# Performance work log

Measured on AMD Instinct MI355X. Metric: run time of the kernel, lower is better.

## Reference

```python
import jax, jax.numpy as jnp
import numpy as np

B, N, S = 2, 16384, 4096
C_FEAT = 6
RADII = (0.5, 1.0)
NSAMPLES = (16, 32)
MLPS = ([9, 16, 16, 32], [9, 32, 32, 64])  # in-channels = 3 (xyz) + 6 (features)
IC, PC, OUT = 64, 96, 128  # image ch, point ch (32+64), fusion out
RC = PC // 4


def _w(key, o, i):
    return jax.random.normal(key, (o, i), jnp.float32) / np.sqrt(i)


def setup_inputs() -> dict:
    key = jax.random.key(0)
    ks = jax.random.split(key, 40)
    inp = {
        "xyz": jax.random.normal(ks[0], (B, N, 3), jnp.float32),
        "features": jax.random.normal(ks[1], (B, C_FEAT, N), jnp.float32),
        "img_features": jax.random.normal(ks[2], (B, IC, S), jnp.float32),
    }
    k = 3
    for s, mlp in enumerate(MLPS):
        for l in range(len(mlp) - 1):
            inp[f"w{s}_{l}"] = _w(ks[k], mlp[l + 1], mlp[l]); k += 1
            inp[f"b{s}_{l}"] = jnp.zeros((mlp[l + 1],), jnp.float32)
    inp["w_img"] = _w(ks[k], PC, IC); k += 1
    inp["b_img"] = jnp.zeros((PC,), jnp.float32)
    inp["w_fc2"] = _w(ks[k], RC, PC); k += 1
    inp["b_fc2"] = jnp.zeros((RC,), jnp.float32)
    inp["w_fc3"] = _w(ks[k], 1, RC); k += 1
    inp["b_fc3"] = jnp.zeros((1,), jnp.float32)
    inp["w_pc"] = _w(ks[k], PC, PC); k += 1
    inp["b_pc"] = jnp.zeros((PC,), jnp.float32)
    inp["w_fuse"] = _w(ks[k], OUT, 2 * PC); k += 1
    inp["b_fuse"] = jnp.zeros((OUT,), jnp.float32)
    return inp


def conv1d(w, b, x):
    # 1x1 Conv1d: w [O,C], x [B,C,N]
    return jnp.einsum('oc,bcn->bon', w, x) + b[None, :, None]


def fps(xyz, npoint):
    # farthest point sampling. xyz: [B,N,3] -> idx [B,npoint]
    b, n, _ = xyz.shape
    first = jnp.zeros((b,), jnp.int32)

    def body(carry, _):
        dists, last = carry
        last_xyz = jnp.take_along_axis(xyz, last[:, None, None].astype(jnp.int32), axis=1)  # [B,1,3]
        d = jnp.sum((xyz - last_xyz) ** 2, -1)  # [B,N]
        dists = jnp.minimum(dists, d)
        nxt = jnp.argmax(dists, -1).astype(jnp.int32)
        return (dists, nxt), nxt

    (_, _), rest = jax.lax.scan(body, (jnp.full((b, n), 1e10, jnp.float32), first), None, length=npoint - 1)
    return jnp.concatenate([first[None, :], rest], 0).T  # [B,npoint]


def ball_query(xyz, new_xyz, radius, nsample):
    # xyz [B,N,3], new_xyz [B,S,3] -> idx [B,S,nsample]
    d2 = jnp.sum((new_xyz[:, :, None, :] - xyz[:, None, :, :]) ** 2, -1)  # [B,S,N]
    ar = jnp.arange(xyz.shape[1], dtype=jnp.int32)
    keys = jnp.where(d2 < radius * radius, ar[None, None, :], xyz.shape[1])
    idx = -jax.lax.top_k(-keys, nsample)[0]  # nsample smallest keys (first in-ball indices)
    first = idx[..., :1]
    idx = jnp.where(idx == xyz.shape[1], first, idx)  # pad with first in-ball index (pointnet2 semantics)
    return jnp.minimum(idx, xyz.shape[1] - 1)


def _forward(xyz, features, img_features, params):
    (w0_0, b0_0, w0_1, b0_1, w0_2, b0_2,
     w1_0, b1_0, w1_1, b1_1, w1_2, b1_2,
     w_img, b_img, w_fc2, b_fc2, w_fc3, b_fc3, w_pc, b_pc, w_fuse, b_fuse) = params
    layers = [[(w0_0, b0_0), (w0_1, b0_1), (w0_2, b0_2)],
              [(w1_0, b1_0), (w1_1, b1_1), (w1_2, b1_2)]]

    fps_idx = fps(xyz, S)  # [B,S]
    new_xyz = jnp.take_along_axis(xyz, fps_idx[:, :, None], axis=1)  # [B,S,3]

    outs = []
    for radius, nsample, mlp in zip(RADII, NSAMPLES, layers):
        idx = ball_query(xyz, new_xyz, radius, nsample)  # [B,S,K]
        g_xyz = jax.vmap(lambda p, i: p[i])(xyz, idx)  # [B,S,K,3]
        g_xyz = (g_xyz - new_xyz[:, :, None, :]).transpose(0, 3, 1, 2)  # [B,3,S,K]
        g_feat = jax.vmap(lambda f, i: f[:, i])(features, idx)  # [B,C,S,K]
        h = jnp.concatenate([g_xyz, g_feat], axis=1)  # [B,3+C,S,K]  (use_xyz)
        for w, b in mlp:
            h = jax.nn.relu(jnp.einsum('oc,bcsk->bosk', w, h) + b[None, :, None, None])
        outs.append(jnp.max(h, axis=-1))  # max-pool over neighborhood -> [B,Cout,S]
    point_feats = jnp.concatenate(outs, axis=1)  # [B,96,S]

    # IA_Layer (BatchNorm at default running stats ~ identity; omitted)
    img = jax.nn.relu(conv1d(w_img, b_img, img_features))  # [B,PC,S]
    flat = img.transpose(0, 2, 1)  # [B,S,PC]
    ri = jnp.tanh(flat @ w_fc2.T + b_fc2)  # [B,S,RC]
    att = jax.nn.sigmoid(ri @ w_fc3.T + b_fc3).transpose(0, 2, 1)  # [B,1,S]
    img_r = img + img * att
    img_new = jax.nn.relu(conv1d(w_pc, b_pc, img_r))  # [B,PC,S]

    fused = jnp.concatenate([point_feats, img_new], axis=1)  # [B,2*PC,S]
    return jax.nn.relu(conv1d(w_fuse, b_fuse, fused))  # [B,OUT,S]


def reference(xyz, features, img_features,
              w0_0, b0_0, w0_1, b0_1, w0_2, b0_2,
              w1_0, b1_0, w1_1, b1_1, w1_2, b1_2,
              w_img, b_img, w_fc2, b_fc2, w_fc3, b_fc3,
              w_pc, b_pc, w_fuse, b_fuse):
    params = (w0_0, b0_0, w0_1, b0_1, w0_2, b0_2,
              w1_0, b1_0, w1_1, b1_1, w1_2, b1_2,
              w_img, b_img, w_fc2, b_fc2, w_fc3, b_fc3, w_pc, b_pc, w_fuse, b_fuse)
    return _forward(xyz, features, img_features, params)
```

## Files before the change

kernel.cpp:

```cpp
#include <hip/hip_runtime.h>
#include <cstdint>

typedef unsigned long long u64;

static constexpr int BB = 2;
static constexpr int NN = 16384;
static constexpr int SS = 4096;

template <int CTRL>
__device__ __forceinline__ u64 dpp_max_step(u64 k) {
  int lo = (int)(unsigned)(k & 0xffffffffull);
  int hi = (int)(unsigned)(k >> 32);
  int slo = __builtin_amdgcn_update_dpp(0, lo, CTRL, 0xF, 0xF, true);
  int shi = __builtin_amdgcn_update_dpp(0, hi, CTRL, 0xF, 0xF, true);
  u64 o = ((u64)(unsigned)shi << 32) | (u64)(unsigned)slo;
  return (o > k) ? o : k;
}

__device__ __forceinline__ unsigned spread4(unsigned v) {
  return (v & 1u) | ((v & 2u) << 2) | ((v & 4u) << 4) | ((v & 8u) << 6);
}

__device__ __forceinline__ unsigned cell_of(float x, float y, float z) {
  int cx = (int)floorf((x + 4.f) * 2.f);
  int cy = (int)floorf((y + 4.f) * 2.f);
  int cz = (int)floorf((z + 4.f) * 2.f);
  cx = min(max(cx, 0), 15); cy = min(max(cy, 0), 15); cz = min(max(cz, 0), 15);
  return spread4((unsigned)cx) | (spread4((unsigned)cy) << 1) |
         (spread4((unsigned)cz) << 2);
}

__global__ __launch_bounds__(1024) void sort_kernel(
    const float* __restrict__ xyz, float4* __restrict__ spts)
{
  const int b = blockIdx.x;
  const float* X = xyz + (size_t)b * NN * 3;
  float4* SP = spts + (size_t)b * NN;
  const int t = threadIdx.x;
  const int lane = t & 63, wid = t >> 6;

  __shared__ unsigned h[4096];
  __shared__ unsigned wtot[16];
  for (int j = t; j < 4096; j += 1024) h[j] = 0;
  __syncthreads();

  for (int i = 0; i < 16; ++i) {
    int p = i * 1024 + t;
    atomicAdd(&h[cell_of(X[p * 3 + 0], X[p * 3 + 1], X[p * 3 + 2])], 1u);
  }
  __syncthreads();

  unsigned a0 = h[4 * t], a1 = h[4 * t + 1], a2 = h[4 * t + 2], a3 = h[4 * t + 3];
  unsigned s4 = a0 + a1 + a2 + a3;
  unsigned incl = s4;
  for (int off = 1; off < 64; off <<= 1) {
    unsigned v = (unsigned)__shfl_up((int)incl, off);
    if (lane >= off) incl += v;
  }
  if (lane == 63) wtot[wid] = incl;
  __syncthreads();
  if (t == 0) {
    unsigned run = 0;
    for (int j = 0; j < 16; ++j) { unsigned tm = wtot[j]; wtot[j] = run; run += tm; }
  }
  __syncthreads();
  unsigned ex = wtot[wid] + (incl - s4);
  h[4 * t] = ex; h[4 * t + 1] = ex + a0;
  h[4 * t + 2] = ex + a0 + a1; h[4 * t + 3] = ex + a0 + a1 + a2;
  __syncthreads();

  for (int i = 0; i < 16; ++i) {
    int p = i * 1024 + t;
    float x = X[p * 3 + 0], y = X[p * 3 + 1], z = X[p * 3 + 2];
    unsigned pos = atomicAdd(&h[cell_of(x, y, z)], 1u);
    SP[pos] = make_float4(x, y, z, __int_as_float(p));
  }
}

__global__ __launch_bounds__(1024) void fps_kernel(
    const float* __restrict__ xyz, const float4* __restrict__ spts,
    float* __restrict__ new_xyz)
{
  const int b = blockIdx.x;
  const float* X = xyz + (size_t)b * NN * 3;
  float* NX = new_xyz + (size_t)b * SS * 3;
  const float4* SP = spts + (size_t)b * NN;
  const int t = threadIdx.x;
  const int lane = t & 63, wid = t >> 6;
  const int g = lane & 3;
  const float4* WP = SP + wid * 1024;

  float x0, x1, x2, x3, x4, x5, x6, x7, x8, x9, x10, x11, x12, x13, x14, x15;
  float y0, y1, y2, y3, y4, y5, y6, y7, y8, y9, y10, y11, y12, y13, y14, y15;
  float z0, z1, z2, z3, z4, z5, z6, z7, z8, z9, z10, z11, z12, z13, z14, z15;
  unsigned n0, n1, n2, n3, n4, n5, n6, n7, n8, n9, n10, n11, n12, n13, n14, n15;
#define LOADSLOT(s)                                                           \
  { float4 P = WP[(s) * 64 + lane];                                           \
    x##s = P.x; y##s = P.y; z##s = P.z; n##s = ~__float_as_uint(P.w); }
  LOADSLOT(0)  LOADSLOT(1)  LOADSLOT(2)  LOADSLOT(3)
  LOADSLOT(4)  LOADSLOT(5)  LOADSLOT(6)  LOADSLOT(7)
  LOADSLOT(8)  LOADSLOT(9)  LOADSLOT(10) LOADSLOT(11)
  LOADSLOT(12) LOADSLOT(13) LOADSLOT(14) LOADSLOT(15)
#undef LOADSLOT

  float d0 = 1e10f, d1 = 1e10f, d2 = 1e10f, d3 = 1e10f,
        d4 = 1e10f, d5 = 1e10f, d6 = 1e10f, d7 = 1e10f,
        d8 = 1e10f, d9 = 1e10f, d10 = 1e10f, d11 = 1e10f,
        d12 = 1e10f, d13 = 1e10f, d14 = 1e10f, d15 = 1e10f;

  float bnx = 0.f, bny = 0.f, bnz = 0.f, bxx = 0.f, bxy = 0.f, bxz = 0.f;
#define SUBBOX(J, A, B, C, D)                                                 \
  {                                                                           \
    float mnx = fminf(fminf(x##A, x##B), fminf(x##C, x##D));                  \
    float mxx = fmaxf(fmaxf(x##A, x##B), fmaxf(x##C, x##D));                  \
    float mny = fminf(fminf(y##A, y##B), fminf(y##C, y##D));                  \
    float mxy = fmaxf(fmaxf(y##A, y##B), fmaxf(y##C, y##D));                  \
    float mnz = fminf(fminf(z##A, z##B), fminf(z##C, z##D));                  \
    float mxz = fmaxf(fmaxf(z##A, z##B), fmaxf(z##C, z##D));                  \
    for (int off = 1; off < 64; off <<= 1) {                                  \
      mnx = fminf(mnx, __shfl_xor(mnx, off));                                 \
      mxx = fmaxf(mxx, __shfl_xor(mxx, off));                                 \
      mny = fminf(mny, __shfl_xor(mny, off));                                 \
      mxy = fmaxf(mxy, __shfl_xor(mxy, off));                                 \
      mnz = fminf(mnz, __shfl_xor(mnz, off));                                 \
      mxz = fmaxf(mxz, __shfl_xor(mxz, off));                                 \
    }                                                                         \
    if (g == J) { bnx = mnx; bny = mny; bnz = mnz;                            \
                  bxx = mxx; bxy = mxy; bxz = mxz; }                          \
  }
  SUBBOX(0, 0, 1, 2, 3)
  SUBBOX(1, 4, 5, 6, 7)
  SUBBOX(2, 8, 9, 10, 11)
  SUBBOX(3, 12, 13, 14, 15)
#undef SUBBOX

  unsigned klo = 0u, khi = __float_as_uint(1e10f);

  __shared__ u64 s_part[2][16];
  int sel = 0;

  for (int it = 1; it < SS; ++it) {
    const float qx = X[sel * 3 + 0];
    const float qy = X[sel * 3 + 1];
    const float qz = X[sel * 3 + 2];
    if (t == 0) {
      NX[(it - 1) * 3 + 0] = qx;
      NX[(it - 1) * 3 + 1] = qy;
      NX[(it - 1) * 3 + 2] = qz;
    }

    float tx = fmaxf(fmaxf(__fsub_rn(bnx, qx), __fsub_rn(qx, bxx)), 0.f);
    float ty = fmaxf(fmaxf(__fsub_rn(bny, qy), __fsub_rn(qy, bxy)), 0.f);
    float tz = fmaxf(fmaxf(__fsub_rn(bnz, qz), __fsub_rn(qz, bxz)), 0.f);
    float lb2 = fmaf(tx, tx, fmaf(ty, ty, __fmul_rn(tz, tz)));
    u64 bm = __ballot(__fmul_rn(lb2, 0.99998474f) < __uint_as_float(khi));
    unsigned m = (unsigned)bm & 0xFu;

#define UPD1(S)                                                               \
    {                                                                         \
      float dx = __fsub_rn(x##S, qx);                                         \
      float dy = __fsub_rn(y##S, qy);                                         \
      float dz = __fsub_rn(z##S, qz);                                         \
      float dsq = __fadd_rn(__fadd_rn(__fmul_rn(dx, dx), __fmul_rn(dy, dy)),  \
                            __fmul_rn(dz, dz));                               \
      d##S = fminf(d##S, dsq);                                                \
      u64 kp = ((u64)__float_as_uint(d##S) << 32) | (u64)(n##S);              \
      if (kp > kb) kb = kp;                                                   \
    }
#define SUBUPD(J, A, B, C, D)                                                 \
    if (m & (1u << J)) {                                                      \
      u64 kb = 0;                                                             \
      UPD1(A) UPD1(B) UPD1(C) UPD1(D)                                         \
      kb = dpp_max_step<0x111>(kb);                                           \
      kb = dpp_max_step<0x112>(kb);                                           \
      kb = dpp_max_step<0x114>(kb);                                           \
      kb = dpp_max_step<0x118>(kb);                                           \
      kb = dpp_max_step<0x142>(kb);                                           \
      kb = dpp_max_step<0x143>(kb);                                           \
      unsigned nlo = (unsigned)__shfl((int)(unsigned)(kb & 0xffffffffull), 63);\
      unsigned nhi = (unsigned)__shfl((int)(unsigned)(kb >> 32), 63);         \
      if (g == J) { klo = nlo; khi = nhi; }                                   \
    }
    SUBUPD(0, 0, 1, 2, 3)
    SUBUPD(1, 4, 5, 6, 7)
    SUBUPD(2, 8, 9, 10, 11)
    SUBUPD(3, 12, 13, 14, 15)
#undef SUBUPD
#undef UPD1

    u64 kw = ((u64)khi << 32) | (u64)klo;
    kw = dpp_max_step<0xB1>(kw);
    kw = dpp_max_step<0x4E>(kw);

    const int pb = it & 1;
    if (lane == 63) s_part[pb][wid] = kw;
    __syncthreads();
    u64 kk = s_part[pb][lane & 15];
    kk = dpp_max_step<0x128>(kk);
    kk = dpp_max_step<0x124>(kk);
    kk = dpp_max_step<0x122>(kk);
    kk = dpp_max_step<0x121>(kk);
    sel = (int)(~(unsigned)(kk & 0xffffffffull));
    sel = __builtin_amdgcn_readfirstlane(sel);
  }
  if (t == 0) {
    NX[(SS - 1) * 3 + 0] = X[sel * 3 + 0];
    NX[(SS - 1) * 3 + 1] = X[sel * 3 + 1];
    NX[(SS - 1) * 3 + 2] = X[sel * 3 + 2];
  }
}

template <int NS>
__global__ __launch_bounds__(256) void ballq_kernel(
    const float* __restrict__ xyz, const float* __restrict__ new_xyz,
    int* __restrict__ out, float r2)
{
  const int q = blockIdx.x * 4 + (threadIdx.x >> 6);
  const int lane = threadIdx.x & 63;
  const int b = q >> 12;
  const float* X = xyz + (size_t)b * NN * 3;
  const float cx = new_xyz[q * 3 + 0];
  const float cy = new_xyz[q * 3 + 1];
  const float cz = new_xyz[q * 3 + 2];
  int* o = out + (size_t)q * NS;
  int base = 0;
  int firstIdx = 0x7fffffff;
  for (int c0 = 0; c0 < NN; c0 += 64) {
    const int p = c0 + lane;
    float dx = __fsub_rn(cx, X[p * 3 + 0]);
    float dy = __fsub_rn(cy, X[p * 3 + 1]);
    float dz = __fsub_rn(cz, X[p * 3 + 2]);
    float d2 = __fadd_rn(__fadd_rn(__fmul_rn(dx, dx), __fmul_rn(dy, dy)),
                         __fmul_rn(dz, dz));
    const bool inb = d2 < r2;
    const unsigned long long mm = __ballot(inb);
    if (inb) {
      int rank = base + (int)__popcll(mm & ((1ull << lane) - 1ull));
      if (rank < NS) {
        o[rank] = p;
        if (rank == 0) firstIdx = p;
      }
    }
    base += (int)__popcll(mm);
    if (base >= NS) break;
  }
#pragma unroll
  for (int off = 32; off >= 1; off >>= 1)
    firstIdx = min(firstIdx, __shfl_xor(firstIdx, off));
  for (int r = base + lane; r < NS; r += 64) o[r] = firstIdx;
}

template <int NS, int C1, int C2, int C3>
__global__ __launch_bounds__(256) void group_mlp_kernel(
    const float* __restrict__ xyz, const float* __restrict__ feat,
    const float* __restrict__ new_xyz, const int* __restrict__ idx,
    const float* __restrict__ w0, const float* __restrict__ b0,
    const float* __restrict__ w1, const float* __restrict__ b1,
    const float* __restrict__ w2, const float* __restrict__ b2,
    float* __restrict__ pf, int chOff)
{
  constexpr int QPB = 256 / NS;
  const int q = blockIdx.x * QPB + (int)(threadIdx.x / NS);
  const int k = (int)(threadIdx.x % NS);
  const int b = q >> 12;
  const int s = q & (SS - 1);
  const float* X = xyz + (size_t)b * NN * 3;
  const float* F = feat + (size_t)b * 6 * NN;
  const int p = idx[(size_t)q * NS + k];

  float in[9];
  in[0] = X[p * 3 + 0] - new_xyz[q * 3 + 0];
  in[1] = X[p * 3 + 1] - new_xyz[q * 3 + 1];
  in[2] = X[p * 3 + 2] - new_xyz[q * 3 + 2];
#pragma unroll
  for (int c = 0; c < 6; ++c) in[3 + c] = F[c * NN + p];

  float h1[C1];
#pragma unroll
  for (int oc = 0; oc < C1; ++oc) {
    float a = b0[oc];
#pragma unroll
    for (int c = 0; c < 9; ++c) a = fmaf(w0[oc * 9 + c], in[c], a);
    h1[oc] = fmaxf(a, 0.f);
  }
  float h2[C2];
#pragma unroll
  for (int oc = 0; oc < C2; ++oc) {
    float a = b1[oc];
#pragma unroll
    for (int c = 0; c < C1; ++c) a = fmaf(w1[oc * C1 + c], h1[c], a);
    h2[oc] = fmaxf(a, 0.f);
  }
#pragma unroll
  for (int oc = 0; oc < C3; ++oc) {
    float a = b2[oc];
#pragma unroll
    for (int c = 0; c < C2; ++c) a = fmaf(w2[oc * C2 + c], h2[c], a);
    float v = fmaxf(a, 0.f);
#pragma unroll
    for (int off = NS / 2; off >= 1; off >>= 1)
      v = fmaxf(v, __shfl_xor(v, off));
    if (k == 0) pf[(((size_t)b * 96) + chOff + oc) * SS + s] = v;
  }
}

__global__ __launch_bounds__(256) void img_fuse_kernel(
    const float* __restrict__ imgf, const float* __restrict__ pf,
    const float* __restrict__ w_img, const float* __restrict__ b_img,
    const float* __restrict__ w_fc2, const float* __restrict__ b_fc2,
    const float* __restrict__ w_fc3, const float* __restrict__ b_fc3,
    const float* __restrict__ w_pc, const float* __restrict__ b_pc,
    const float* __restrict__ w_fuse, const float* __restrict__ b_fuse,
    float* __restrict__ out)
{
  constexpr int TS = 32;
  __shared__ float x_lds[64][TS];
  __shared__ float img_lds[96][TS];
  __shared__ float ri_lds[24][TS];
  __shared__ float att_lds[TS];
  __shared__ float imgn_lds[96][TS];
  __shared__ float pf_lds[96][TS];

  const int blk = blockIdx.x;
  const int b = blk / (SS / TS);
  const int s0 = (blk % (SS / TS)) * TS;
  const int tid = threadIdx.x;

  for (int i = tid; i < 64 * TS; i += 256) {
    int c = i / TS, s = i % TS;
    x_lds[c][s] = imgf[((size_t)b * 64 + c) * SS + s0 + s];
  }
  for (int i = tid; i < 96 * TS; i += 256) {
    int c = i / TS, s = i % TS;
    pf_lds[c][s] = pf[((size_t)b * 96 + c) * SS + s0 + s];
  }
  __syncthreads();

  for (int i = tid; i < 96 * TS; i += 256) {
    int oc = i / TS, s = i % TS;
    float a = b_img[oc];
#pragma unroll
    for (int c = 0; c < 64; ++c) a = fmaf(w_img[oc * 64 + c], x_lds[c][s], a);
    img_lds[oc][s] = fmaxf(a, 0.f);
  }
  __syncthreads();

  for (int i = tid; i < 24 * TS; i += 256) {
    int r = i / TS, s = i % TS;
    float a = b_fc2[r];
#pragma unroll
    for (int c = 0; c < 96; ++c) a = fmaf(w_fc2[r * 96 + c], img_lds[c][s], a);
    ri_lds[r][s] = tanhf(a);
  }
  __syncthreads();

  if (tid < TS) {
    float a = b_fc3[0];
#pragma unroll
    for (int r = 0; r < 24; ++r) a = fmaf(w_fc3[r], ri_lds[r][tid], a);
    att_lds[tid] = 1.f / (1.f + expf(-a));
  }
  __syncthreads();

  for (int i = tid; i < 96 * TS; i += 256) {
    int c = i / TS, s = i % TS;
    float v = img_lds[c][s];
    img_lds[c][s] = fmaf(v, att_lds[s], v);
  }
  __syncthreads();

  for (int i = tid; i < 96 * TS; i += 256) {
    int oc = i / TS, s = i % TS;
    float a = b_pc[oc];
#pragma unroll
    for (int c = 0; c < 96; ++c) a = fmaf(w_pc[oc * 96 + c], img_lds[c][s], a);
    imgn_lds[oc][s] = fmaxf(a, 0.f);
  }
  __syncthreads();

  for (int i = tid; i < 128 * TS; i += 256) {
    int oc = i / TS, s = i % TS;
    float a = b_fuse[oc];
#pragma unroll
    for (int c = 0; c < 96; ++c) a = fmaf(w_fuse[oc * 192 + c], pf_lds[c][s], a);
#pragma unroll
    for (int c = 0; c < 96; ++c) a = fmaf(w_fuse[oc * 192 + 96 + c], imgn_lds[c][s], a);
    out[((size_t)b * 128 + oc) * SS + s0 + s] = fmaxf(a, 0.f);
  }
}

extern "C" void kernel_launch(void* const* d_in, const int* in_sizes, int n_in,
                              void* d_out, int out_size, void* d_ws, size_t ws_size,
                              hipStream_t stream)
{
  const float* xyz    = (const float*)d_in[0];
  const float* feat   = (const float*)d_in[1];
  const float* imgf   = (const float*)d_in[2];
  const float* w0_0   = (const float*)d_in[3];
  const float* b0_0   = (const float*)d_in[4];
  const float* w0_1   = (const float*)d_in[5];
  const float* b0_1   = (const float*)d_in[6];
  const float* w0_2   = (const float*)d_in[7];
  const float* b0_2   = (const float*)d_in[8];
  const float* w1_0   = (const float*)d_in[9];
  const float* b1_0   = (const float*)d_in[10];
  const float* w1_1   = (const float*)d_in[11];
  const float* b1_1   = (const float*)d_in[12];
  const float* w1_2   = (const float*)d_in[13];
  const float* b1_2   = (const float*)d_in[14];
  const float* w_img  = (const float*)d_in[15];
  const float* b_img  = (const float*)d_in[16];
  const float* w_fc2  = (const float*)d_in[17];
  const float* b_fc2  = (const float*)d_in[18];
  const float* w_fc3  = (const float*)d_in[19];
  const float* b_fc3  = (const float*)d_in[20];
  const float* w_pc   = (const float*)d_in[21];
  const float* b_pc   = (const float*)d_in[22];
  const float* w_fuse = (const float*)d_in[23];
  const float* b_fuse = (const float*)d_in[24];
  float* out = (float*)d_out;

  float4* spts = (float4*)d_ws;
  float*  nxyz = (float*)(spts + (size_t)BB * NN);
  int*    idx0 = (int*)(nxyz + (size_t)BB * SS * 3);
  int*    idx1 = idx0 + (size_t)BB * SS * 16;
  float*  pf   = (float*)(idx1 + (size_t)BB * SS * 32);

  sort_kernel<<<BB, 1024, 0, stream>>>(xyz, spts);
  fps_kernel<<<BB, 1024, 0, stream>>>(xyz, spts, nxyz);
  ballq_kernel<16><<<BB * SS / 4, 256, 0, stream>>>(xyz, nxyz, idx0, 0.25f);
  ballq_kernel<32><<<BB * SS / 4, 256, 0, stream>>>(xyz, nxyz, idx1, 1.0f);
  group_mlp_kernel<16, 16, 16, 32><<<BB * SS / 16, 256, 0, stream>>>(
      xyz, feat, nxyz, idx0, w0_0, b0_0, w0_1, b0_1, w0_2, b0_2, pf, 0);
  group_mlp_kernel<32, 32, 32, 64><<<BB * SS / 8, 256, 0, stream>>>(
      xyz, feat, nxyz, idx1, w1_0, b1_0, w1_1, b1_1, w1_2, b1_2, pf, 32);
  img_fuse_kernel<<<BB * SS / 32, 256, 0, stream>>>(
      imgf, pf, w_img, b_img, w_fc2, b_fc2, w_fc3, b_fc3, w_pc, b_pc,
      w_fuse, b_fuse, out);
}
```

Baseline: 4.629 ms.

## Halve FPS block to 8 waves with packed float2 distance math

The FPS kernel now runs 512 threads (8 waves) per batch, with each lane holding 32 points stored as float2 pairs so the compiler can issue packed FP32 ops. Points are grouped into 8 sub-boxes instead of 4. The 64-bit DPP argmax is replaced by two 32-bit wave max reductions: one over distance, then one over index among the lanes that hit that max. This cuts the per-iteration barrier and the cross-wave reduction to 8 entries, at the cost of a longer serial chain per wave, higher register pressure and fewer active waves.

```diff
diff --git a/kernel.cpp b/kernel.cpp
--- a/kernel.cpp
+++ b/kernel.cpp
@@ -2,6 +2,7 @@
 #include <cstdint>
 
 typedef unsigned long long u64;
+typedef float v2f __attribute__((ext_vector_type(2)));
 
 static constexpr int BB = 2;
 static constexpr int NN = 16384;
@@ -17,6 +18,28 @@
   return (o > k) ? o : k;
 }
 
+__device__ __forceinline__ unsigned wave_umax_bcast(unsigned v) {
+  unsigned o;
+#define WSTEP(C)                                                              \
+  o = (unsigned)__builtin_amdgcn_update_dpp(0, (int)v, C, 0xF, 0xF, true);   \
+  v = (o > v) ? o : v;
+  WSTEP(0x111)
+  WSTEP(0x112)
+  WSTEP(0x114)
+  WSTEP(0x118)
+  WSTEP(0x142)
+  WSTEP(0x143)
+#undef WSTEP
+  return (unsigned)__builtin_amdgcn_readlane((int)v, 63);
+}
+
+__device__ __forceinline__ v2f emin2(v2f a, v2f b) {
+  v2f r; r[0] = fminf(a[0], b[0]); r[1] = fminf(a[1], b[1]); return r;
+}
+__device__ __forceinline__ v2f emax2(v2f a, v2f b) {
+  v2f r; r[0] = fmaxf(a[0], b[0]); r[1] = fmaxf(a[1], b[1]); return r;
+}
+
 __device__ __forceinline__ unsigned spread4(unsigned v) {
   return (v & 1u) | ((v & 2u) << 2) | ((v & 4u) << 4) | ((v & 8u) << 6);
 }
@@ -77,46 +100,57 @@
   }
 }
 
-__global__ __launch_bounds__(1024) void fps_kernel(
+__global__ __launch_bounds__(512, 2) void fps_kernel(
     const float* __restrict__ xyz, const float4* __restrict__ spts,
     float* __restrict__ new_xyz)
 {
+#pragma clang fp contract(off)
   const int b = blockIdx.x;
   const float* X = xyz + (size_t)b * NN * 3;
   float* NX = new_xyz + (size_t)b * SS * 3;
   const float4* SP = spts + (size_t)b * NN;
   const int t = threadIdx.x;
   const int lane = t & 63, wid = t >> 6;
-  const int g = lane & 3;
-  const float4* WP = SP + wid * 1024;
-
-  float x0, x1, x2, x3, x4, x5, x6, x7, x8, x9, x10, x11, x12, x13, x14, x15;
-  float y0, y1, y2, y3, y4, y5, y6, y7, y8, y9, y10, y11, y12, y13, y14, y15;
-  float z0, z1, z2, z3, z4, z5, z6, z7, z8, z9, z10, z11, z12, z13, z14, z15;
-  unsigned n0, n1, n2, n3, n4, n5, n6, n7, n8, n9, n10, n11, n12, n13, n14, n15;
-#define LOADSLOT(s)                                                           \
-  { float4 P = WP[(s) * 64 + lane];                                           \
-    x##s = P.x; y##s = P.y; z##s = P.z; n##s = ~__float_as_uint(P.w); }
-  LOADSLOT(0)  LOADSLOT(1)  LOADSLOT(2)  LOADSLOT(3)
-  LOADSLOT(4)  LOADSLOT(5)  LOADSLOT(6)  LOADSLOT(7)
-  LOADSLOT(8)  LOADSLOT(9)  LOADSLOT(10) LOADSLOT(11)
-  LOADSLOT(12) LOADSLOT(13) LOADSLOT(14) LOADSLOT(15)
-#undef LOADSLOT
-
-  float d0 = 1e10f, d1 = 1e10f, d2 = 1e10f, d3 = 1e10f,
-        d4 = 1e10f, d5 = 1e10f, d6 = 1e10f, d7 = 1e10f,
-        d8 = 1e10f, d9 = 1e10f, d10 = 1e10f, d11 = 1e10f,
-        d12 = 1e10f, d13 = 1e10f, d14 = 1e10f, d15 = 1e10f;
+  const float4* WP = SP + wid * 2048;
+
+  v2f xp0, xp1, xp2, xp3, xp4, xp5, xp6, xp7,
+      xp8, xp9, xp10, xp11, xp12, xp13, xp14, xp15;
+  v2f yp0, yp1, yp2, yp3, yp4, yp5, yp6, yp7,
+      yp8, yp9, yp10, yp11, yp12, yp13, yp14, yp15;
+  v2f zp0, zp1, zp2, zp3, zp4, zp5, zp6, zp7,
+      zp8, zp9, zp10, zp11, zp12, zp13, zp14, zp15;
+  v2f dp0, dp1, dp2, dp3, dp4, dp5, dp6, dp7,
+      dp8, dp9, dp10, dp11, dp12, dp13, dp14, dp15;
+  unsigned na0, na1, na2, na3, na4, na5, na6, na7,
+           na8, na9, na10, na11, na12, na13, na14, na15;
+  unsigned nb0, nb1, nb2, nb3, nb4, nb5, nb6, nb7,
+           nb8, nb9, nb10, nb11, nb12, nb13, nb14, nb15;
+
+#define LOADV(v)                                                              \
+  {                                                                           \
+    float4 Pa = WP[(2 * (v)) * 64 + lane];                                    \
+    float4 Pb = WP[(2 * (v) + 1) * 64 + lane];                                \
+    xp##v[0] = Pa.x; xp##v[1] = Pb.x;                                         \
+    yp##v[0] = Pa.y; yp##v[1] = Pb.y;                                         \
+    zp##v[0] = Pa.z; zp##v[1] = Pb.z;                                         \
+    na##v = ~__float_as_uint(Pa.w); nb##v = ~__float_as_uint(Pb.w);           \
+    dp##v[0] = 1e10f; dp##v[1] = 1e10f;                                       \
+  }
+  LOADV(0)  LOADV(1)  LOADV(2)  LOADV(3)
+  LOADV(4)  LOADV(5)  LOADV(6)  LOADV(7)
+  LOADV(8)  LOADV(9)  LOADV(10) LOADV(11)
+  LOADV(12) LOADV(13) LOADV(14) LOADV(15)
+#undef LOADV
 
   float bnx = 0.f, bny = 0.f, bnz = 0.f, bxx = 0.f, bxy = 0.f, bxz = 0.f;
-#define SUBBOX(J, A, B, C, D)                                                 \
+#define SUBBOX(J, A, B)                                                       \
   {                                                                           \
-    float mnx = fminf(fminf(x##A, x##B), fminf(x##C, x##D));                  \
-    float mxx = fmaxf(fmaxf(x##A, x##B), fmaxf(x##C, x##D));                  \
-    float mny = fminf(fminf(y##A, y##B), fminf(y##C, y##D));                  \
-    float mxy = fmaxf(fmaxf(y##A, y##B), fmaxf(y##C, y##D));                  \
-    float mnz = fminf(fminf(z##A, z##B), fminf(z##C, z##D));                  \
-    float mxz = fmaxf(fmaxf(z##A, z##B), fmaxf(z##C, z##D));                  \
+    v2f nv = emin2(xp##A, xp##B), xv = emax2(xp##A, xp##B);                   \
+    float mnx = fminf(nv[0], nv[1]), mxx = fmaxf(xv[0], xv[1]);               \
+    nv = emin2(yp##A, yp##B); xv = emax2(yp##A, yp##B);                       \
+    float mny = fminf(nv[0], nv[1]), mxy = fmaxf(xv[0], xv[1]);               \
+    nv = emin2(zp##A, zp##B); xv = emax2(zp##A, zp##B);                       \
+    float mnz = fminf(nv[0], nv[1]), mxz = fmaxf(xv[0], xv[1]);               \
     for (int off = 1; off < 64; off <<= 1) {                                  \
       mnx = fminf(mnx, __shfl_xor(mnx, off));                                 \
       mxx = fmaxf(mxx, __shfl_xor(mxx, off));                                 \
@@ -125,18 +159,16 @@
       mnz = fminf(mnz, __shfl_xor(mnz, off));                                 \
       mxz = fmaxf(mxz, __shfl_xor(mxz, off));                                 \
     }                                                                         \
-    if (g == J) { bnx = mnx; bny = mny; bnz = mnz;                            \
-                  bxx = mxx; bxy = mxy; bxz = mxz; }                          \
-  }
-  SUBBOX(0, 0, 1, 2, 3)
-  SUBBOX(1, 4, 5, 6, 7)
-  SUBBOX(2, 8, 9, 10, 11)
-  SUBBOX(3, 12, 13, 14, 15)
+    if ((lane & 7) == J) { bnx = mnx; bny = mny; bnz = mnz;                   \
+                           bxx = mxx; bxy = mxy; bxz = mxz; }                 \
+  }
+  SUBBOX(0, 0, 1)   SUBBOX(1, 2, 3)   SUBBOX(2, 4, 5)   SUBBOX(3, 6, 7)
+  SUBBOX(4, 8, 9)   SUBBOX(5, 10, 11) SUBBOX(6, 12, 13) SUBBOX(7, 14, 15)
 #undef SUBBOX
 
-  unsigned klo = 0u, khi = __float_as_uint(1e10f);
-
-  __shared__ u64 s_part[2][16];
+  unsigned wkhi = __float_as_uint(1e10f), wklo = 0u;
+
+  __shared__ u64 s_part[2][8];
   int sel = 0;
 
   for (int it = 1; it < SS; ++it) {
@@ -148,55 +180,49 @@
       NX[(it - 1) * 3 + 1] = qy;
       NX[(it - 1) * 3 + 2] = qz;
     }
+    v2f q2x, q2y, q2z;
+    q2x[0] = qx; q2x[1] = qx;
+    q2y[0] = qy; q2y[1] = qy;
+    q2z[0] = qz; q2z[1] = qz;
 
     float tx = fmaxf(fmaxf(__fsub_rn(bnx, qx), __fsub_rn(qx, bxx)), 0.f);
     float ty = fmaxf(fmaxf(__fsub_rn(bny, qy), __fsub_rn(qy, bxy)), 0.f);
     float tz = fmaxf(fmaxf(__fsub_rn(bnz, qz), __fsub_rn(qz, bxz)), 0.f);
     float lb2 = fmaf(tx, tx, fmaf(ty, ty, __fmul_rn(tz, tz)));
-    u64 bm = __ballot(__fmul_rn(lb2, 0.99998474f) < __uint_as_float(khi));
-    unsigned m = (unsigned)bm & 0xFu;
-
-#define UPD1(S)                                                               \
-    {                                                                         \
-      float dx = __fsub_rn(x##S, qx);                                         \
-      float dy = __fsub_rn(y##S, qy);                                         \
-      float dz = __fsub_rn(z##S, qz);                                         \
-      float dsq = __fadd_rn(__fadd_rn(__fmul_rn(dx, dx), __fmul_rn(dy, dy)),  \
-                            __fmul_rn(dz, dz));                               \
-      d##S = fminf(d##S, dsq);                                                \
-      u64 kp = ((u64)__float_as_uint(d##S) << 32) | (u64)(n##S);              \
-      if (kp > kb) kb = kp;                                                   \
+    u64 bm = __ballot(__fmul_rn(lb2, 0.99998474f) < __uint_as_float(wkhi));
+    unsigned m = (unsigned)bm & 0xFFu;
+
+#define SUBUPD(J, A, B)                                                       \
+    if (m & (1u << J)) {                                                      \
+      v2f dxA = xp##A - q2x, dyA = yp##A - q2y, dzA = zp##A - q2z;            \
+      v2f sA = (dxA * dxA + dyA * dyA) + dzA * dzA;                           \
+      dp##A = emin2(dp##A, sA);                                               \
+      v2f dxB = xp##B - q2x, dyB = yp##B - q2y, dzB = zp##B - q2z;            \
+      v2f sB = (dxB * dxB + dyB * dyB) + dzB * dzB;                           \
+      dp##B = emin2(dp##B, sB);                                               \
+      v2f mv = emax2(dp##A, dp##B);                                           \
+      unsigned mm = __float_as_uint(fmaxf(mv[0], mv[1]));                     \
+      mm = wave_umax_bcast(mm);                                               \
+      unsigned c0 = (__float_as_uint(dp##A[0]) == mm) ? na##A : 0u;           \
+      unsigned c1 = (__float_as_uint(dp##A[1]) == mm) ? nb##A : 0u;           \
+      unsigned c2 = (__float_as_uint(dp##B[0]) == mm) ? na##B : 0u;           \
+      unsigned c3 = (__float_as_uint(dp##B[1]) == mm) ? nb##B : 0u;           \
+      unsigned cc = wave_umax_bcast(max(max(c0, c1), max(c2, c3)));           \
+      if ((lane & 7) == J) { wkhi = mm; wklo = cc; }                          \
     }
-#define SUBUPD(J, A, B, C, D)                                                 \
-    if (m & (1u << J)) {                                                      \
-      u64 kb = 0;                                                             \
-      UPD1(A) UPD1(B) UPD1(C) UPD1(D)                                         \
-      kb = dpp_max_step<0x111>(kb);                                           \
-      kb = dpp_max_step<0x112>(kb);                                           \
-      kb = dpp_max_step<0x114>(kb);                                           \
-      kb = dpp_max_step<0x118>(kb);                                           \
-      kb = dpp_max_step<0x142>(kb);                                           \
-      kb = dpp_max_step<0x143>(kb);                                           \
-      unsigned nlo = (unsigned)__shfl((int)(unsigned)(kb & 0xffffffffull), 63);\
-      unsigned nhi = (unsigned)__shfl((int)(unsigned)(kb >> 32), 63);         \
-      if (g == J) { klo = nlo; khi = nhi; }                                   \
-    }
-    SUBUPD(0, 0, 1, 2, 3)
-    SUBUPD(1, 4, 5, 6, 7)
-    SUBUPD(2, 8, 9, 10, 11)
-    SUBUPD(3, 12, 13, 14, 15)
+    SUBUPD(0, 0, 1)   SUBUPD(1, 2, 3)   SUBUPD(2, 4, 5)   SUBUPD(3, 6, 7)
+    SUBUPD(4, 8, 9)   SUBUPD(5, 10, 11) SUBUPD(6, 12, 13) SUBUPD(7, 14, 15)
 #undef SUBUPD
-#undef UPD1
-
-    u64 kw = ((u64)khi << 32) | (u64)klo;
-    kw = dpp_max_step<0xB1>(kw);
-    kw = dpp_max_step<0x4E>(kw);
+
+    u64 kw = ((u64)wkhi << 32) | (u64)wklo;
+    kw = dpp_max_step<0x124>(kw);
+    kw = dpp_max_step<0x122>(kw);
+    kw = dpp_max_step<0x121>(kw);
 
     const int pb = it & 1;
-    if (lane == 63) s_part[pb][wid] = kw;
+    if (lane == 0) s_part[pb][wid] = kw;
     __syncthreads();
-    u64 kk = s_part[pb][lane & 15];
-    kk = dpp_max_step<0x128>(kk);
+    u64 kk = s_part[pb][lane & 7];
     kk = dpp_max_step<0x124>(kk);
     kk = dpp_max_step<0x122>(kk);
     kk = dpp_max_step<0x121>(kk);
@@ -427,7 +453,7 @@
   float*  pf   = (float*)(idx1 + (size_t)BB * SS * 32);
 
   sort_kernel<<<BB, 1024, 0, stream>>>(xyz, spts);
-  fps_kernel<<<BB, 1024, 0, stream>>>(xyz, spts, nxyz);
+  fps_kernel<<<BB, 512, 0, stream>>>(xyz, spts, nxyz);
   ballq_kernel<16><<<BB * SS / 4, 256, 0, stream>>>(xyz, nxyz, idx0, 0.25f);
   ballq_kernel<32><<<BB * SS / 4, 256, 0, stream>>>(xyz, nxyz, idx1, 1.0f);
   group_mlp_kernel<16, 16, 16, 32><<<BB * SS / 16, 256, 0, stream>>>(
```

New measurement: 5.189 ms. +12.1%, slower.
